# Performance work log

Measured on AMD Instinct MI355X. Metric: run time of the kernel, lower is better.

Reference implementation:

```python
import jax, jax.numpy as jnp
import numpy as np

N, D, E = 10000, 64, 32768   # nodes, padded degree, target edges
F, H, O = 64, 256, 1         # in_channels, hidden_channels, out_channels


def _linear_init(key, fin, fout):
    kw, kb = jax.random.split(key)
    s = 1.0 / np.sqrt(fin)
    w = jax.random.uniform(kw, (fin, fout), jnp.float32, -s, s)
    b = jax.random.uniform(kb, (fout,), jnp.float32, -s, s)
    return w, b


def setup_inputs() -> dict:
    key = jax.random.key(0)
    ks = jax.random.split(key, 12)
    x = jax.random.normal(ks[0], (N, F), jnp.float32)
    adj_nbr = jax.random.randint(ks[1], (N, D), 0, N)          # padded neighbor lists
    tar_ei = jax.random.randint(ks[2], (2, E), 0, N)           # target edges
    xcn_w1, xcn_b1 = _linear_init(ks[3], F, H)
    xcn_w2, xcn_b2 = _linear_init(ks[4], H, H)
    xcn_w3, xcn_b3 = _linear_init(ks[5], H, H)
    xij_w1, xij_b1 = _linear_init(ks[6], F, H)
    xij_w2, xij_b2 = _linear_init(ks[7], H, H)
    lin_w1, lin_b1 = _linear_init(ks[8], H, H)
    lin_w2, lin_b2 = _linear_init(ks[9], H, O)
    beta = jnp.ones((1,), jnp.float32)
    return dict(x=x, adj_nbr=adj_nbr, tar_ei=tar_ei, beta=beta,
                xcn_w1=xcn_w1, xcn_b1=xcn_b1, xcn_w2=xcn_w2, xcn_b2=xcn_b2,
                xcn_w3=xcn_w3, xcn_b3=xcn_b3,
                xij_w1=xij_w1, xij_b1=xij_b1, xij_w2=xij_w2, xij_b2=xij_b2,
                lin_w1=lin_w1, lin_b1=lin_b1, lin_w2=lin_w2, lin_b2=lin_b2)


def reference(x, adj_nbr, tar_ei, beta,
              xcn_w1, xcn_b1, xcn_w2, xcn_b2, xcn_w3, xcn_b3,
              xij_w1, xij_b1, xij_w2, xij_b2,
              lin_w1, lin_b1, lin_w2, lin_b2):
    relu = jax.nn.relu
    i, j = tar_ei[0], tar_ei[1]
    # adjoverlap: common-neighbor intersection of rows i and j of the adjacency
    ni = adj_nbr[i]                                   # [E, D] neighbors of i
    nj = adj_nbr[j]                                   # [E, D] neighbors of j
    cm = (ni[:, :, None] == nj[:, None, :]).any(-1)   # [E, D] ni[a] in N(j)?
    # spmm_add(cn, x): sum features of common neighbors per target edge
    xcn = jnp.einsum('ed,edf->ef', cm.astype(x.dtype), x[ni])  # [E, F]
    # xijlin(xi * xj): Linear -> ReLU -> Linear
    xij = x[i] * x[j]
    h_ij = relu(xij @ xij_w1 + xij_b1) @ xij_w2 + xij_b2
    # xcnlin(xcn): Linear -> ReLU -> Linear -> ReLU -> Linear
    h_cn = relu(xcn @ xcn_w1 + xcn_b1)
    h_cn = relu(h_cn @ xcn_w2 + xcn_b2)
    h_cn = h_cn @ xcn_w3 + xcn_b3
    # lin(xcnlin(xcn) * beta + xij): Linear -> ReLU -> Linear
    h = relu((h_cn * beta + h_ij) @ lin_w1 + lin_b1)
    return h @ lin_w2 + lin_b2                        # [E, O]
```

## Files before the change

### kernel.cpp

```cpp
#include <hip/hip_runtime.h>

#define NNODES 10000
#define DDEG   64
#define NEDGES 32768
#define FIN    64
#define HID    256

typedef __attribute__((ext_vector_type(8))) __bf16 bf16x8;
typedef __attribute__((ext_vector_type(4))) float  f32x4;

__device__ __forceinline__ unsigned short f2bf(float f) {
    unsigned x = __float_as_uint(f);
    return (unsigned short)((x + 0x7FFFu + ((x >> 16) & 1u)) >> 16);
}
__device__ __forceinline__ float b2f(unsigned short u) {
    return __uint_as_float(((unsigned)u) << 16);
}

#define OFF_XIJ1 0
#define OFF_XIJ2 16384
#define OFF_XCN1 81920
#define OFF_XCN2 98304
#define OFF_XCN3 163840
#define OFF_LIN1 229376
#define WT_TOTAL 294912
#define NTILES   36
#define NSS_ALL  18

__host__ __device__ constexpr int tile_off(int t) {
    return t < 2  ? OFF_XIJ1 + t * 8192
         : t < 10 ? OFF_XIJ2 + (t - 2) * 8192
         : t < 12 ? OFF_XCN1 + (t - 10) * 8192
         : t < 20 ? OFF_XCN2 + (t - 12) * 8192
         : t < 28 ? OFF_XCN3 + (t - 20) * 8192
         :          OFF_LIN1 + (t - 28) * 8192;
}

__device__ __forceinline__ void gll16(const unsigned short* g, unsigned short* l) {
    __builtin_amdgcn_global_load_lds(
        (const __attribute__((address_space(1))) unsigned int*)g,
        (__attribute__((address_space(3))) unsigned int*)l, 16, 0, 0);
}
__device__ __forceinline__ void stage_tile(const unsigned short* g, unsigned short* l,
                                           int tid, int wv) {
#pragma unroll
    for (int c = 0; c < 2; ++c)
        gll16(g + c * 4096 + tid * 8, l + c * 4096 + wv * 512);
}
__device__ __forceinline__ void stage_pair(const unsigned short* __restrict__ WT, int g,
                                           unsigned short* ring, int tid, int wv) {
    const unsigned short* src = WT + tile_off(2 * g);
    unsigned short* dst = ring + ((2 * g) & 3) * 8192;
#pragma unroll
    for (int c = 0; c < 4; ++c)
        gll16(src + c * 4096 + tid * 8, dst + c * 4096 + wv * 512);
}

__global__ __launch_bounds__(256) void edge_prep_k(const float* __restrict__ x,
                                                   const int* __restrict__ adj,
                                                   const int* __restrict__ tar,
                                                   const float* __restrict__ xij_w1,
                                                   const float* __restrict__ xij_w2,
                                                   const float* __restrict__ xcn_w1,
                                                   const float* __restrict__ xcn_w2,
                                                   const float* __restrict__ xcn_w3,
                                                   const float* __restrict__ lin_w1,
                                                   unsigned short* __restrict__ WT,
                                                   unsigned short* __restrict__ xij_g,
                                                   unsigned short* __restrict__ xcn_g) {
    const int wv   = threadIdx.x >> 6;
    const int lane = threadIdx.x & 63;
    const int e    = blockIdx.x * 4 + wv;

    int i = tar[e];
    int j = tar[NEDGES + e];
    int ni = adj[i * DDEG + lane];
    int nj = adj[j * DDEG + lane];
    float xi = x[i * FIN + lane];
    float xj = x[j * FIN + lane];

    bool found = false;
#pragma unroll
    for (int b = 0; b < 64; ++b)
        found |= (ni == (int)__builtin_amdgcn_readlane(nj, b));
    unsigned long long m = __ballot(found);

    float acc = 0.f;
    while (m) {
        int a = __ffsll(m) - 1;
        m &= m - 1;
        int r = (int)__builtin_amdgcn_readlane(ni, a);
        acc += x[r * FIN + lane];
    }
    int sl = lane ^ ((e & 7) << 3);
    xij_g[(size_t)e * FIN + sl] = f2bf(xi * xj);
    xcn_g[(size_t)e * FIN + sl] = f2bf(acc);

    if (blockIdx.x < WT_TOTAL / 256) {
        int idx = blockIdx.x * 256 + threadIdx.x;
        const float* src;
        int r;
        if (idx < OFF_XIJ2)      { r = idx - OFF_XIJ1; src = xij_w1; }
        else if (idx < OFF_XCN1) { r = idx - OFF_XIJ2; src = xij_w2; }
        else if (idx < OFF_XCN2) { r = idx - OFF_XCN1; src = xcn_w1; }
        else if (idx < OFF_XCN3) { r = idx - OFF_XCN2; src = xcn_w2; }
        else if (idx < OFF_LIN1) { r = idx - OFF_XCN3; src = xcn_w3; }
        else                     { r = idx - OFF_LIN1; src = lin_w1; }
        int kb  = r >> 13;
        int n   = (r & 8191) >> 5;
        int klo = r & 31;
        WT[idx] = f2bf(src[(kb * 32 + klo) * HID + n]);
    }
}

template <int G0, int NSS, int LDA>
__device__ __forceinline__ void run_phase(const unsigned short* As,
                                          unsigned short* ring,
                                          const unsigned short* __restrict__ WT,
                                          const unsigned short* __restrict__ restage_src,
                                          unsigned short* sX,
                                          int lr, int lg, int col0, int r0,
                                          int tid, int wv, f32x4 acc[4][4]) {
#pragma unroll
    for (int m = 0; m < 4; ++m)
#pragma unroll
        for (int n = 0; n < 4; ++n) acc[m][n] = (f32x4){0.f, 0.f, 0.f, 0.f};
    const int sw = (lr & 7) << 3;
#pragma unroll
    for (int ss = 0; ss < NSS; ++ss) {
        const int g = G0 + ss;
        asm volatile("s_waitcnt vmcnt(0) lgkmcnt(0)" ::: "memory");
        __builtin_amdgcn_s_barrier();
        if (g + 1 < NSS_ALL)
            stage_pair(WT, g + 1, ring, tid, wv);
        if (restage_src && ss == 0)
            stage_tile(restage_src, sX, tid, wv);
#pragma unroll
        for (int half = 0; half < 2; ++half) {
            const int t  = 2 * g + half;
            const int kk = (ss * 2 + half) * 32;
            const unsigned short* cur = ring + (t & 3) * 8192;
            bf16x8 a[4], b[4];
#pragma unroll
            for (int n = 0; n < 4; ++n)
                b[n] = *reinterpret_cast<const bf16x8*>(&cur[(col0 + n * 16 + lr) * 32 + 8 * lg]);
#pragma unroll
            for (int m = 0; m < 4; ++m)
                a[m] = *reinterpret_cast<const bf16x8*>(
                    &As[(r0 + m * 16 + lr) * LDA + ((kk + 8 * lg) ^ sw)]);
            __builtin_amdgcn_s_setprio(1);
#pragma unroll
            for (int m = 0; m < 4; ++m)
#pragma unroll
                for (int n = 0; n < 4; ++n)
                    acc[m][n] = __builtin_amdgcn_mfma_f32_16x16x32_bf16(a[m], b[n], acc[m][n], 0, 0, 0);
            __builtin_amdgcn_s_setprio(0);
        }
    }
}

__global__ __launch_bounds__(512, 1) void mlp_k(const unsigned short* __restrict__ xij_g,
                                                const unsigned short* __restrict__ xcn_g,
                                                const unsigned short* __restrict__ WT,
                                                unsigned* __restrict__ hij_g,
                                                const float* __restrict__ xij_b1,
                                                const float* __restrict__ xij_b2,
                                                const float* __restrict__ xcn_b1,
                                                const float* __restrict__ xcn_b2,
                                                const float* __restrict__ xcn_b3,
                                                const float* __restrict__ lin_b1,
                                                const float* __restrict__ lin_w2,
                                                const float* __restrict__ lin_b2,
                                                const float* __restrict__ beta,
                                                float* __restrict__ out) {
    __shared__ unsigned short sX[128 * 64];
    __shared__ unsigned short sH[128 * 256];
    __shared__ unsigned short sB[4 * 8192];

    const int tid  = threadIdx.x;
    const int wv   = tid >> 6;
    const int lane = tid & 63;
    const int lr   = lane & 15;
    const int lg   = lane >> 4;
    const int r0   = (wv >> 2) * 64;
    const int col0 = (wv & 3) * 64;
    const int row0 = blockIdx.x * 128;

    stage_tile(xij_g + (size_t)row0 * FIN, sX, tid, wv);
    stage_pair(WT, 0, sB, tid, wv);
    const float betaf = beta[0];
    unsigned* hbase = hij_g + (size_t)(blockIdx.x * 8 + wv) * 2048 + lane * 2;

    f32x4 acc[4][4];
    float bl[4];

    run_phase<0, 1, 64>(sX, sB, WT, nullptr, nullptr, lr, lg, col0, r0, tid, wv, acc);
#pragma unroll
    for (int n = 0; n < 4; ++n) bl[n] = xij_b1[col0 + n * 16 + lr];
#pragma unroll
    for (int m = 0; m < 4; ++m)
#pragma unroll
        for (int n = 0; n < 4; ++n)
#pragma unroll
            for (int i = 0; i < 4; ++i) {
                int row = r0 + m * 16 + 4 * lg + i;
                int col = col0 + n * 16 + lr;
                sH[row * HID + (col ^ ((row & 7) << 3))] = f2bf(fmaxf(acc[m][n][i] + bl[n], 0.f));
            }

    run_phase<1, 4, 256>(sH, sB, WT, xcn_g + (size_t)row0 * FIN, sX, lr, lg, col0, r0, tid, wv, acc);
#pragma unroll
    for (int n = 0; n < 4; ++n) bl[n] = xij_b2[col0 + n * 16 + lr];
#pragma unroll
    for (int m = 0; m < 4; ++m)
#pragma unroll
        for (int n = 0; n < 4; ++n) {
            uint2 v;
            v.x = ((unsigned)f2bf(acc[m][n][1] + bl[n]) << 16) | f2bf(acc[m][n][0] + bl[n]);
            v.y = ((unsigned)f2bf(acc[m][n][3] + bl[n]) << 16) | f2bf(acc[m][n][2] + bl[n]);
            *reinterpret_cast<uint2*>(hbase + (m * 4 + n) * 128) = v;
        }

    run_phase<5, 1, 64>(sX, sB, WT, nullptr, nullptr, lr, lg, col0, r0, tid, wv, acc);
#pragma unroll
    for (int n = 0; n < 4; ++n) bl[n] = xcn_b1[col0 + n * 16 + lr];
#pragma unroll
    for (int m = 0; m < 4; ++m)
#pragma unroll
        for (int n = 0; n < 4; ++n)
#pragma unroll
            for (int i = 0; i < 4; ++i) {
                int row = r0 + m * 16 + 4 * lg + i;
                int col = col0 + n * 16 + lr;
                sH[row * HID + (col ^ ((row & 7) << 3))] = f2bf(fmaxf(acc[m][n][i] + bl[n], 0.f));
            }

    run_phase<6, 4, 256>(sH, sB, WT, nullptr, nullptr, lr, lg, col0, r0, tid, wv, acc);
    asm volatile("s_waitcnt lgkmcnt(0)" ::: "memory");
    __builtin_amdgcn_s_barrier();
#pragma unroll
    for (int n = 0; n < 4; ++n) bl[n] = xcn_b2[col0 + n * 16 + lr];
#pragma unroll
    for (int m = 0; m < 4; ++m)
#pragma unroll
        for (int n = 0; n < 4; ++n)
#pragma unroll
            for (int i = 0; i < 4; ++i) {
                int row = r0 + m * 16 + 4 * lg + i;
                int col = col0 + n * 16 + lr;
                sH[row * HID + (col ^ ((row & 7) << 3))] = f2bf(fmaxf(acc[m][n][i] + bl[n], 0.f));
            }

    run_phase<10, 4, 256>(sH, sB, WT, nullptr, nullptr, lr, lg, col0, r0, tid, wv, acc);
    asm volatile("s_waitcnt lgkmcnt(0)" ::: "memory");
    __builtin_amdgcn_s_barrier();
#pragma unroll
    for (int n = 0; n < 4; ++n) bl[n] = xcn_b3[col0 + n * 16 + lr];
#pragma unroll
    for (int m = 0; m < 4; ++m)
#pragma unroll
        for (int n = 0; n < 4; ++n) {
            uint2 v = *reinterpret_cast<const uint2*>(hbase + (m * 4 + n) * 128);
            float h0 = b2f((unsigned short)(v.x & 0xFFFF));
            float h1 = b2f((unsigned short)(v.x >> 16));
            float h2 = b2f((unsigned short)(v.y & 0xFFFF));
            float h3 = b2f((unsigned short)(v.y >> 16));
            float v0 = (acc[m][n][0] + bl[n]) * betaf + h0;
            float v1 = (acc[m][n][1] + bl[n]) * betaf + h1;
            float v2 = (acc[m][n][2] + bl[n]) * betaf + h2;
            float v3 = (acc[m][n][3] + bl[n]) * betaf + h3;
            int rb = r0 + m * 16 + 4 * lg;
            int col = col0 + n * 16 + lr;
            sH[(rb + 0) * HID + (col ^ (((rb + 0) & 7) << 3))] = f2bf(v0);
            sH[(rb + 1) * HID + (col ^ (((rb + 1) & 7) << 3))] = f2bf(v1);
            sH[(rb + 2) * HID + (col ^ (((rb + 2) & 7) << 3))] = f2bf(v2);
            sH[(rb + 3) * HID + (col ^ (((rb + 3) & 7) << 3))] = f2bf(v3);
        }

    run_phase<14, 4, 256>(sH, sB, WT, nullptr, nullptr, lr, lg, col0, r0, tid, wv, acc);
#pragma unroll
    for (int n = 0; n < 4; ++n) bl[n] = lin_b1[col0 + n * 16 + lr];
    float w2l[4];
#pragma unroll
    for (int n = 0; n < 4; ++n) w2l[n] = lin_w2[col0 + n * 16 + lr];
    float* sRed = (float*)sX;
#pragma unroll
    for (int m = 0; m < 4; ++m) {
        float p[4] = {0.f, 0.f, 0.f, 0.f};
#pragma unroll
        for (int n = 0; n < 4; ++n)
#pragma unroll
            for (int i = 0; i < 4; ++i)
                p[i] += fmaxf(acc[m][n][i] + bl[n], 0.f) * w2l[n];
#pragma unroll
        for (int i = 0; i < 4; ++i) {
            float s = p[i];
            s += __shfl_xor(s, 1);
            s += __shfl_xor(s, 2);
            s += __shfl_xor(s, 4);
            s += __shfl_xor(s, 8);
            if (lr == 0) sRed[(wv & 3) * 128 + r0 + m * 16 + 4 * lg + i] = s;
        }
    }
    __syncthreads();
    if (tid < 128)
        out[row0 + tid] = sRed[tid] + sRed[128 + tid] + sRed[256 + tid] + sRed[384 + tid] + lin_b2[0];
}

extern "C" void kernel_launch(void* const* d_in, const int* in_sizes, int n_in,
                              void* d_out, int out_size, void* d_ws, size_t ws_size,
                              hipStream_t stream) {
    const float* x      = (const float*)d_in[0];
    const int*   adj    = (const int*)d_in[1];
    const int*   tar    = (const int*)d_in[2];
    const float* beta   = (const float*)d_in[3];
    const float* xcn_w1 = (const float*)d_in[4];
    const float* xcn_b1 = (const float*)d_in[5];
    const float* xcn_w2 = (const float*)d_in[6];
    const float* xcn_b2 = (const float*)d_in[7];
    const float* xcn_w3 = (const float*)d_in[8];
    const float* xcn_b3 = (const float*)d_in[9];
    const float* xij_w1 = (const float*)d_in[10];
    const float* xij_b1 = (const float*)d_in[11];
    const float* xij_w2 = (const float*)d_in[12];
    const float* xij_b2 = (const float*)d_in[13];
    const float* lin_w1 = (const float*)d_in[14];
    const float* lin_b1 = (const float*)d_in[15];
    const float* lin_w2 = (const float*)d_in[16];
    const float* lin_b2 = (const float*)d_in[17];

    unsigned short* WT    = (unsigned short*)d_ws;
    unsigned short* xij_g = (unsigned short*)((char*)d_ws + 589824);
    unsigned short* xcn_g = (unsigned short*)((char*)d_ws + 4784128);
    unsigned*       hij_g = (unsigned*)((char*)d_ws + 8978432);

    edge_prep_k<<<NEDGES / 4, 256, 0, stream>>>(x, adj, tar,
                                                xij_w1, xij_w2, xcn_w1, xcn_w2, xcn_w3, lin_w1,
                                                WT, xij_g, xcn_g);
    mlp_k<<<NEDGES / 128, 512, 0, stream>>>(xij_g, xcn_g, WT, hij_g,
                                            xij_b1, xij_b2, xcn_b1, xcn_b2, xcn_b3,
                                            lin_b1, lin_w2, lin_b2, beta, (float*)d_out);
}
```

Baseline: 59.25 us.

## Pipeline weight tiles one at a time with three-deep prefetch and partial waits

The weight staging changes from pairs of tiles with a full vmcnt(0) wait per pair to single tiles prefetched three ahead in the 4-slot ring. Partial waits (vmcnt(4)/vmcnt(2)) let later loads stay in flight while the current tile is consumed. This hides more global-to-LDS latency behind MFMA work. The cost is twice as many barriers per phase, plus an extra fence barrier before the last phase.

```diff
diff --git a/kernel.cpp b/kernel.cpp
--- a/kernel.cpp
+++ b/kernel.cpp
@@ -25,7 +25,6 @@
 #define OFF_LIN1 229376
 #define WT_TOTAL 294912
 #define NTILES   36
-#define NSS_ALL  18
 
 __host__ __device__ constexpr int tile_off(int t) {
     return t < 2  ? OFF_XIJ1 + t * 8192
@@ -41,19 +40,11 @@
         (const __attribute__((address_space(1))) unsigned int*)g,
         (__attribute__((address_space(3))) unsigned int*)l, 16, 0, 0);
 }
-__device__ __forceinline__ void stage_tile(const unsigned short* g, unsigned short* l,
-                                           int tid, int wv) {
+__device__ __forceinline__ void stage16(const unsigned short* g, unsigned short* l,
+                                        int tid, int wv) {
 #pragma unroll
     for (int c = 0; c < 2; ++c)
         gll16(g + c * 4096 + tid * 8, l + c * 4096 + wv * 512);
-}
-__device__ __forceinline__ void stage_pair(const unsigned short* __restrict__ WT, int g,
-                                           unsigned short* ring, int tid, int wv) {
-    const unsigned short* src = WT + tile_off(2 * g);
-    unsigned short* dst = ring + ((2 * g) & 3) * 8192;
-#pragma unroll
-    for (int c = 0; c < 4; ++c)
-        gll16(src + c * 4096 + tid * 8, dst + c * 4096 + wv * 512);
 }
 
 __global__ __launch_bounds__(256) void edge_prep_k(const float* __restrict__ x,
@@ -113,7 +104,7 @@
     }
 }
 
-template <int G0, int NSS, int LDA>
+template <int T0, int NT, int LDA, bool RESTAGE>
 __device__ __forceinline__ void run_phase(const unsigned short* As,
                                           unsigned short* ring,
                                           const unsigned short* __restrict__ WT,
@@ -127,36 +118,41 @@
         for (int n = 0; n < 4; ++n) acc[m][n] = (f32x4){0.f, 0.f, 0.f, 0.f};
     const int sw = (lr & 7) << 3;
 #pragma unroll
-    for (int ss = 0; ss < NSS; ++ss) {
-        const int g = G0 + ss;
-        asm volatile("s_waitcnt vmcnt(0) lgkmcnt(0)" ::: "memory");
+    for (int s = 0; s < NT; ++s) {
+        const int t = T0 + s;
+        if (t <= NTILES - 3)
+            asm volatile("s_waitcnt vmcnt(4) lgkmcnt(0)" ::: "memory");
+        else if (t == NTILES - 2)
+            asm volatile("s_waitcnt vmcnt(2) lgkmcnt(0)" ::: "memory");
+        else
+            asm volatile("s_waitcnt vmcnt(0) lgkmcnt(0)" ::: "memory");
         __builtin_amdgcn_s_barrier();
-        if (g + 1 < NSS_ALL)
-            stage_pair(WT, g + 1, ring, tid, wv);
-        if (restage_src && ss == 0)
-            stage_tile(restage_src, sX, tid, wv);
-#pragma unroll
-        for (int half = 0; half < 2; ++half) {
-            const int t  = 2 * g + half;
-            const int kk = (ss * 2 + half) * 32;
-            const unsigned short* cur = ring + (t & 3) * 8192;
-            bf16x8 a[4], b[4];
+        if (t + 3 < NTILES)
+            stage16(WT + tile_off(t + 3), ring + ((t + 3) & 3) * 8192, tid, wv);
+        if (RESTAGE && s == 0)
+            stage16(restage_src, sX, tid, wv);
+        const unsigned short* cur = ring + (t & 3) * 8192;
+        bf16x8 a[4], b[4];
+#pragma unroll
+        for (int n = 0; n < 4; ++n)
+            b[n] = *reinterpret_cast<const bf16x8*>(&cur[(col0 + n * 16 + lr) * 32 + 8 * lg]);
+#pragma unroll
+        for (int m = 0; m < 4; ++m)
+            a[m] = *reinterpret_cast<const bf16x8*>(
+                &As[(r0 + m * 16 + lr) * LDA + ((s * 32 + 8 * lg) ^ sw)]);
+        __builtin_amdgcn_s_setprio(1);
+#pragma unroll
+        for (int m = 0; m < 4; ++m)
 #pragma unroll
             for (int n = 0; n < 4; ++n)
-                b[n] = *reinterpret_cast<const bf16x8*>(&cur[(col0 + n * 16 + lr) * 32 + 8 * lg]);
-#pragma unroll
-            for (int m = 0; m < 4; ++m)
-                a[m] = *reinterpret_cast<const bf16x8*>(
-                    &As[(r0 + m * 16 + lr) * LDA + ((kk + 8 * lg) ^ sw)]);
-            __builtin_amdgcn_s_setprio(1);
-#pragma unroll
-            for (int m = 0; m < 4; ++m)
-#pragma unroll
-                for (int n = 0; n < 4; ++n)
-                    acc[m][n] = __builtin_amdgcn_mfma_f32_16x16x32_bf16(a[m], b[n], acc[m][n], 0, 0, 0);
-            __builtin_amdgcn_s_setprio(0);
-        }
+                acc[m][n] = __builtin_amdgcn_mfma_f32_16x16x32_bf16(a[m], b[n], acc[m][n], 0, 0, 0);
+        __builtin_amdgcn_s_setprio(0);
     }
+}
+
+__device__ __forceinline__ void fence_barrier() {
+    asm volatile("s_waitcnt lgkmcnt(0)" ::: "memory");
+    __builtin_amdgcn_s_barrier();
 }
 
 __global__ __launch_bounds__(512, 1) void mlp_k(const unsigned short* __restrict__ xij_g,
@@ -186,15 +182,17 @@
     const int col0 = (wv & 3) * 64;
     const int row0 = blockIdx.x * 128;
 
-    stage_tile(xij_g + (size_t)row0 * FIN, sX, tid, wv);
-    stage_pair(WT, 0, sB, tid, wv);
+    stage16(xij_g + (size_t)row0 * FIN, sX, tid, wv);
+    stage16(WT + tile_off(0), sB, tid, wv);
+    stage16(WT + tile_off(1), sB + 8192, tid, wv);
+    stage16(WT + tile_off(2), sB + 16384, tid, wv);
     const float betaf = beta[0];
     unsigned* hbase = hij_g + (size_t)(blockIdx.x * 8 + wv) * 2048 + lane * 2;
 
     f32x4 acc[4][4];
     float bl[4];
 
-    run_phase<0, 1, 64>(sX, sB, WT, nullptr, nullptr, lr, lg, col0, r0, tid, wv, acc);
+    run_phase<0, 2, 64, false>(sX, sB, WT, nullptr, nullptr, lr, lg, col0, r0, tid, wv, acc);
 #pragma unroll
     for (int n = 0; n < 4; ++n) bl[n] = xij_b1[col0 + n * 16 + lr];
 #pragma unroll
@@ -208,7 +206,8 @@
                 sH[row * HID + (col ^ ((row & 7) << 3))] = f2bf(fmaxf(acc[m][n][i] + bl[n], 0.f));
             }
 
-    run_phase<1, 4, 256>(sH, sB, WT, xcn_g + (size_t)row0 * FIN, sX, lr, lg, col0, r0, tid, wv, acc);
+    run_phase<2, 8, 256, true>(sH, sB, WT, xcn_g + (size_t)row0 * FIN, sX,
+                               lr, lg, col0, r0, tid, wv, acc);
 #pragma unroll
     for (int n = 0; n < 4; ++n) bl[n] = xij_b2[col0 + n * 16 + lr];
 #pragma unroll
@@ -221,7 +220,7 @@
             *reinterpret_cast<uint2*>(hbase + (m * 4 + n) * 128) = v;
         }
 
-    run_phase<5, 1, 64>(sX, sB, WT, nullptr, nullptr, lr, lg, col0, r0, tid, wv, acc);
+    run_phase<10, 2, 64, false>(sX, sB, WT, nullptr, nullptr, lr, lg, col0, r0, tid, wv, acc);
 #pragma unroll
     for (int n = 0; n < 4; ++n) bl[n] = xcn_b1[col0 + n * 16 + lr];
 #pragma unroll
@@ -235,9 +234,8 @@
                 sH[row * HID + (col ^ ((row & 7) << 3))] = f2bf(fmaxf(acc[m][n][i] + bl[n], 0.f));
             }
 
-    run_phase<6, 4, 256>(sH, sB, WT, nullptr, nullptr, lr, lg, col0, r0, tid, wv, acc);
-    asm volatile("s_waitcnt lgkmcnt(0)" ::: "memory");
-    __builtin_amdgcn_s_barrier();
+    run_phase<12, 8, 256, false>(sH, sB, WT, nullptr, nullptr, lr, lg, col0, r0, tid, wv, acc);
+    fence_barrier();
 #pragma unroll
     for (int n = 0; n < 4; ++n) bl[n] = xcn_b2[col0 + n * 16 + lr];
 #pragma unroll
@@ -251,9 +249,8 @@
                 sH[row * HID + (col ^ ((row & 7) << 3))] = f2bf(fmaxf(acc[m][n][i] + bl[n], 0.f));
             }
 
-    run_phase<10, 4, 256>(sH, sB, WT, nullptr, nullptr, lr, lg, col0, r0, tid, wv, acc);
-    asm volatile("s_waitcnt lgkmcnt(0)" ::: "memory");
-    __builtin_amdgcn_s_barrier();
+    run_phase<20, 8, 256, false>(sH, sB, WT, nullptr, nullptr, lr, lg, col0, r0, tid, wv, acc);
+    fence_barrier();
 #pragma unroll
     for (int n = 0; n < 4; ++n) bl[n] = xcn_b3[col0 + n * 16 + lr];
 #pragma unroll
@@ -276,8 +273,9 @@
             sH[(rb + 2) * HID + (col ^ (((rb + 2) & 7) << 3))] = f2bf(v2);
             sH[(rb + 3) * HID + (col ^ (((rb + 3) & 7) << 3))] = f2bf(v3);
         }
-
-    run_phase<14, 4, 256>(sH, sB, WT, nullptr, nullptr, lr, lg, col0, r0, tid, wv, acc);
+    fence_barrier();
+
+    run_phase<28, 8, 256, false>(sH, sB, WT, nullptr, nullptr, lr, lg, col0, r0, tid, wv, acc);
 #pragma unroll
     for (int n = 0; n < 4; ++n) bl[n] = lin_b1[col0 + n * 16 + lr];
     float w2l[4];
```

Result: no change. 59.99 us (+1.2%).
